# Optimization experiments

Hardware: AMD Instinct MI355X
Metric: run time of the kernel (lower is better)

Reference implementation:

```python
import jax, jax.numpy as jnp
import numpy as np

B, S, D = 2, 2048, 2048
H, KV = 16, 4
HD = D // H          # 128
QPK = H // KV        # queries per kv head


def setup_inputs() -> dict:
    key = jax.random.key(0)
    ks = jax.random.split(key, 8)
    x = jax.random.normal(ks[0], (B, S, D), jnp.float32)
    mask = jnp.zeros((1, 1, S, S), jnp.float32)  # unused (causal flash path)
    # RoPE tables: theta=10000, shape (S, HD//2)
    inv_freq = 1.0 / (10000.0 ** (jnp.arange(0, HD, 2, dtype=jnp.float32) / HD))
    freqs = jnp.outer(jnp.arange(S, dtype=jnp.float32), inv_freq)
    freqs_cos, freqs_sin = jnp.cos(freqs), jnp.sin(freqs)
    sc = 0.02
    Wq = jax.random.normal(ks[1], (D, H * HD), jnp.float32) * sc
    bq = jnp.zeros((H * HD,), jnp.float32)
    Wk = jax.random.normal(ks[2], (D, KV * HD), jnp.float32) * sc
    bk = jnp.zeros((KV * HD,), jnp.float32)
    Wv = jax.random.normal(ks[3], (D, KV * HD), jnp.float32) * sc
    bv = jnp.zeros((KV * HD,), jnp.float32)
    Wo = jax.random.normal(ks[4], (D, D), jnp.float32) * sc  # bias=False
    return dict(x=x, mask=mask, freqs_cos=freqs_cos, freqs_sin=freqs_sin,
                Wq=Wq, bq=bq, Wk=Wk, bk=bk, Wv=Wv, bv=bv, Wo=Wo)


def _rope(t, cos, sin):
    # t: [B, S, nH, HD]; interleaved-pair rotation as in apply_rope
    tr = t.reshape(t.shape[:-1] + (-1, 2))
    r, i = tr[..., 0], tr[..., 1]
    c = cos[None, :, None, :]
    s = sin[None, :, None, :]
    out = jnp.stack([r * c - i * s, r * s + i * c], axis=-1)
    return out.reshape(t.shape)


def reference(x, mask, freqs_cos, freqs_sin, Wq, bq, Wk, bk, Wv, bv, Wo):
    b, s, d = x.shape
    q = (x @ Wq + bq).reshape(b, s, H, HD)
    k = (x @ Wk + bk).reshape(b, s, KV, HD)
    v = (x @ Wv + bv).reshape(b, s, KV, HD)
    cos, sin = freqs_cos[:s], freqs_sin[:s]
    q = _rope(q, cos, sin)
    k = _rope(k, cos, sin)
    # GQA: repeat_interleave kv heads to match query heads
    k = jnp.repeat(k, QPK, axis=2)
    v = jnp.repeat(v, QPK, axis=2)
    q = q.transpose(0, 2, 1, 3)  # [B, H, S, HD]
    k = k.transpose(0, 2, 1, 3)
    v = v.transpose(0, 2, 1, 3)
    scores = jnp.einsum('bhqd,bhkd->bhqk', q, k) / jnp.sqrt(jnp.float32(HD))
    causal = jnp.tril(jnp.ones((s, s), bool))
    scores = jnp.where(causal[None, None], scores, jnp.finfo(scores.dtype).min)
    attn = jax.nn.softmax(scores, axis=-1)
    out = jnp.einsum('bhqk,bhkd->bhqd', attn, v)
    out = out.transpose(0, 2, 1, 3).reshape(b, s, d)
    return out @ Wo
```

## Files before the change

kernel.cpp:

```cpp
#include <hip/hip_runtime.h>


#define B_  2
#define S_  2048
#define D_  2048
#define H_  16
#define KV_ 4
#define HD_ 128
#define NQK 2560

typedef unsigned short ushort_t;
typedef __attribute__((ext_vector_type(8))) __bf16 bf16x8;
typedef __attribute__((ext_vector_type(4))) float  f32x4;

__device__ __forceinline__ ushort_t f2bf(float f) {
    unsigned u = __float_as_uint(f);
    u += 0x7FFFu + ((u >> 16) & 1u);
    return (ushort_t)(u >> 16);
}
__device__ __forceinline__ ushort_t f2bf_fast(float f) {
    __bf16 h = (__bf16)f;
    return *(ushort_t*)&h;
}
__device__ __forceinline__ float bf2f(ushort_t h) {
    return __uint_as_float(((unsigned)h) << 16);
}

__device__ __forceinline__ void g2l16(const void* g, void* l) {
    __builtin_amdgcn_global_load_lds(
        (const __attribute__((address_space(1))) unsigned int*)g,
        (__attribute__((address_space(3))) unsigned int*)l, 16, 0, 0);
}

#define SOFTSC 0.12751743f


__global__ __launch_bounds__(256) void k_prep(
    const float* __restrict__ x,  ushort_t* __restrict__ xb,
    const float* __restrict__ Wq, const float* __restrict__ Wk,
    const float* __restrict__ Wv, const float* __restrict__ Wo,
    ushort_t* __restrict__ Wt, ushort_t* __restrict__ Wot,
    const float* __restrict__ bq, const float* __restrict__ bk,
    const float* __restrict__ bv, float* __restrict__ bb) {
    __shared__ float tile[32][33];
    int id = blockIdx.x, t = threadIdx.x;
    if (id < 8192) {
        int i = id * 256 + t;
        float4 v = ((const float4*)x)[i];
        ushort4 o;
        o.x = f2bf(v.x); o.y = f2bf(v.y); o.z = f2bf(v.z); o.w = f2bf(v.w);
        ((ushort4*)xb)[i] = o;
        return;
    }
    const float* src; ushort_t* dst; int C, bid;
    if (id < 12288)      { src = Wq; dst = Wt;                       C = 2048; bid = id - 8192;  }
    else if (id < 13312) { src = Wk; dst = Wt + (size_t)2048 * 2048; C = 512;  bid = id - 12288; }
    else if (id < 14336) { src = Wv; dst = Wt + (size_t)2560 * 2048; C = 512;  bid = id - 13312; }
    else if (id < 18432) { src = Wo; dst = Wot;                      C = 2048; bid = id - 14336; }
    else {
        int i = (id - 18432) * 256 + t;
        if (i < 3072)
            bb[i] = (i < 2048) ? bq[i] : (i < 2560) ? bk[i - 2048] : bv[i - 2560];
        return;
    }
    const int R = 2048;
    int nbc = C >> 5;
    int c0 = (bid % nbc) * 32, r0 = (bid / nbc) * 32;
    int tx = t & 31, ty = t >> 5;
    for (int i = ty; i < 32; i += 8)
        tile[i][tx] = src[(size_t)(r0 + i) * C + c0 + tx];
    __syncthreads();
    for (int i = ty; i < 32; i += 8)
        dst[(size_t)(c0 + i) * R + r0 + tx] = f2bf(tile[tx][i]);
}


template<int BK>
__global__ __launch_bounds__(256, 3) void k_gemm(const ushort_t* __restrict__ A,
                                                 const ushort_t* __restrict__ Bt,
                                                 void* __restrict__ Cp,
                                                 const float* __restrict__ bias,
                                                 const float* __restrict__ fc,
                                                 const float* __restrict__ fs,
                                                 ushort_t* __restrict__ Vt,
                                                 int M, int N, int K, int out_bf16) {
    constexpr int GPR    = BK / 8;
    constexpr int RPR    = 64 / GPR;
    constexpr int ROUNDS = 32 / RPR;
    __shared__ __align__(16) ushort_t As[128 * BK];
    __shared__ __align__(16) ushort_t Bs[128 * BK];
    int t = threadIdx.x;
    int w = t >> 6, lane = t & 63, quad = lane >> 4, l16 = lane & 15;
    int L = blockIdx.x;
    int mper = (M >> 7) >> 3;
    int xcd = L & 7, j = L >> 3;
    int m0 = (xcd * mper + (j % mper)) * 128;
    int n0 = (j / mper) * 128;
    int wm = (w >> 1) * 64, wn = (w & 1) * 64;
    f32x4 acc[4][4] = {};

    int rlo = lane / GPR;
    int gsl = lane & (GPR - 1);
    const ushort_t* Ag = A  + (size_t)(m0 + w * 32) * K;
    const ushort_t* Bg = Bt + (size_t)(n0 + w * 32) * K;
    int rsw = (l16 & 7);

    for (int k0 = 0; k0 < K; k0 += BK) {
        __syncthreads();
#pragma unroll
        for (int p = 0; p < ROUNDS; p++) {
            int row = p * RPR + rlo;
            int gs = gsl ^ (row & 7);
            g2l16(Ag + (size_t)row * K + k0 + gs * 8, (char*)As + (w * 32 + p * RPR) * 2 * BK);
            g2l16(Bg + (size_t)row * K + k0 + gs * 8, (char*)Bs + (w * 32 + p * RPR) * 2 * BK);
        }
        __syncthreads();
#pragma unroll
        for (int kc = 0; kc < BK / 32; kc++) {
            int gg = quad + kc * 4;
            bf16x8 af[4], bfr[4];
#pragma unroll
            for (int i = 0; i < 4; i++)
                af[i] = *(const bf16x8*)(As + (wm + i * 16 + l16) * BK + ((gg ^ rsw) * 8));
#pragma unroll
            for (int j2 = 0; j2 < 4; j2++)
                bfr[j2] = *(const bf16x8*)(Bs + (wn + j2 * 16 + l16) * BK + ((gg ^ rsw) * 8));
#pragma unroll
            for (int i = 0; i < 4; i++)
#pragma unroll
                for (int j2 = 0; j2 < 4; j2++)
                    acc[i][j2] = __builtin_amdgcn_mfma_f32_16x16x32_bf16(af[i], bfr[j2], acc[i][j2], 0, 0, 0);
        }
    }
    int ostride = fc ? NQK : N;
#pragma unroll
    for (int i = 0; i < 4; i++) {
        int r = m0 + wm + i * 16 + quad * 4;
#pragma unroll
        for (int j2 = 0; j2 < 4; j2++) {
            int c = n0 + wn + j2 * 16 + l16;
            float bv_ = bias ? bias[c] : 0.f;
            if (fc && c >= 2560) {
                ushort4 pack;
                pack.x = f2bf(acc[i][j2][0] + bv_);
                pack.y = f2bf(acc[i][j2][1] + bv_);
                pack.z = f2bf(acc[i][j2][2] + bv_);
                pack.w = f2bf(acc[i][j2][3] + bv_);
                int kv = (c - 2560) >> 7, d = (c - 2560) & 127;
                int b = r >> 11, s0 = r & (S_ - 1);
                *(ushort4*)&Vt[(((size_t)b * KV_ + kv) * HD_ + d) * S_ + s0] = pack;
                continue;
            }
#pragma unroll
            for (int jr = 0; jr < 4; jr++) {
                float v = acc[i][j2][jr] + bv_;
                if (fc) {
                    int s  = (r + jr) & (S_ - 1);
                    int dp = (c & 127) >> 1;
                    float cs = fc[s * 64 + dp], sn = fs[s * 64 + dp];
                    float p = __shfl_xor(v, 1);
                    v = (c & 1) ? (v * cs + p * sn) : (v * cs - p * sn);
                }
                if (out_bf16) ((ushort_t*)Cp)[(size_t)(r + jr) * ostride + c] = f2bf(v);
                else          ((float*)Cp)[(size_t)(r + jr) * ostride + c] = v;
            }
        }
    }
}


#define G1_K  2048
#define G1_NT 32

__global__ __launch_bounds__(512, 2) void k_gemm1_256(
    const ushort_t* __restrict__ A, const ushort_t* __restrict__ Bt,
    ushort_t* __restrict__ C, const float* __restrict__ bias,
    const float* __restrict__ fc, const float* __restrict__ fs,
    ushort_t* __restrict__ Vt) {
    __shared__ __align__(16) ushort_t As[2][16384];
    __shared__ __align__(16) ushort_t Bs[2][12288];
    int t = threadIdx.x;
    int w = t >> 6, lane = t & 63, quad = lane >> 4, l16 = lane & 15;
    int wm_i = w >> 2, wn_i = w & 3;

    int L = blockIdx.x;
    int xcd = L & 7, j = L >> 3;
    int m0 = (xcd * 2 + (j & 1)) * 256;
    int n0 = (j >> 1) * 192;

    int srow = w * 16 + (lane >> 3);
    int sg   = (lane & 7) ^ (lane >> 3);
    const ushort_t* Ag  = A  + (size_t)(m0 + srow) * G1_K + sg * 8;
    const ushort_t* Bg3 = Bt + (size_t)(n0 + w * 8 + (lane >> 3)) * G1_K + sg * 8;

    int swz = l16 & 7;
    int cA = (quad ^ swz) * 8;
    int cB = ((quad + 4) ^ swz) * 8;

    f32x4 acc[8][3] = {};
    bf16x8 afr[4][2], bfr[3][2];

#define ST1A(KT, HA, BUF) do {                                                  \
    const ushort_t* s_ = Ag + (size_t)(HA) * 128 * G1_K + (KT) * 64;            \
    char* d_ = (char*)&As[BUF][(HA) * 8192] + w * 2048;                         \
    g2l16(s_, d_); g2l16(s_ + 8 * G1_K, d_ + 1024); } while (0)
#define ST1B(KT, G, BUF) do {                                                   \
    const ushort_t* s_ = Bg3 + (size_t)(G) * 64 * G1_K + (KT) * 64;             \
    char* d_ = (char*)&Bs[BUF][(G) * 4096] + w * 1024;                          \
    g2l16(s_, d_); } while (0)

#define RDA1(MH, BUF) do {                                                      \
    const ushort_t* Ar = &As[BUF][(wm_i * 128 + (MH) * 64 + l16) * 64];         \
    _Pragma("unroll") for (int ii = 0; ii < 4; ii++) {                          \
        afr[ii][0] = *(const bf16x8*)(Ar + ii * 1024 + cA);                     \
        afr[ii][1] = *(const bf16x8*)(Ar + ii * 1024 + cB); } } while (0)
#define RDB1(G, BUF) do {                                                       \
    const ushort_t* Br = &Bs[BUF][(wn_i * 48 + (G) * 16 + l16) * 64];           \
    bfr[G][0] = *(const bf16x8*)(Br + cA);                                      \
    bfr[G][1] = *(const bf16x8*)(Br + cB); } while (0)

#define MMA1(MH, G) do {                                                        \
    _Pragma("unroll") for (int kc = 0; kc < 2; kc++)                            \
    _Pragma("unroll") for (int ii = 0; ii < 4; ii++)                            \
        acc[(MH)*4+ii][G] = __builtin_amdgcn_mfma_f32_16x16x32_bf16(            \
            afr[ii][kc], bfr[G][kc], acc[(MH)*4+ii][G], 0, 0, 0); } while (0)

#define BAR1() __builtin_amdgcn_s_barrier()
#define WGK1() do { asm volatile("s_waitcnt lgkmcnt(0)" ::: "memory");          \
                    __builtin_amdgcn_sched_barrier(0); } while (0)

#define TILE1(KT, BUF, OTH) do {                                                \
                                                                        \
    RDA1(0, BUF); RDB1(0, BUF);                                                 \
    if ((KT) + 1 < G1_NT) ST1A((KT) + 1, 0, OTH);                               \
    BAR1(); WGK1();                                                             \
    __builtin_amdgcn_s_setprio(1); MMA1(0, 0); __builtin_amdgcn_s_setprio(0);   \
    BAR1();                                                                     \
                                                                        \
    RDB1(1, BUF); RDB1(2, BUF);                                                 \
    if ((KT) + 1 < G1_NT) ST1A((KT) + 1, 1, OTH);                               \
    BAR1(); WGK1();                                                             \
    __builtin_amdgcn_s_setprio(1); MMA1(0, 1); MMA1(0, 2);                      \
    __builtin_amdgcn_s_setprio(0);                                              \
    BAR1();                                                                     \
          \
    RDA1(1, BUF);                                                               \
    if ((KT) + 2 < G1_NT) { ST1B((KT) + 2, 0, BUF); ST1B((KT) + 2, 1, BUF); }   \
    BAR1(); WGK1();                                                             \
    __builtin_amdgcn_s_setprio(1); MMA1(1, 2); MMA1(1, 1);                      \
    __builtin_amdgcn_s_setprio(0);                                              \
    BAR1();                                                                     \
                              \
    if ((KT) + 2 < G1_NT) ST1B((KT) + 2, 2, BUF);                               \
    if ((KT) < G1_NT - 2) asm volatile("s_waitcnt vmcnt(3)" ::: "memory");      \
    else                  asm volatile("s_waitcnt vmcnt(0)" ::: "memory");      \
    BAR1();                                                                     \
    __builtin_amdgcn_sched_barrier(0);                                          \
    __builtin_amdgcn_s_setprio(1); MMA1(1, 0); __builtin_amdgcn_s_setprio(0);   \
    BAR1();                                                                     \
} while (0)

    ST1B(0, 0, 0); ST1B(0, 1, 0); ST1B(0, 2, 0);
    ST1A(0, 0, 0); ST1A(0, 1, 0);
    ST1B(1, 0, 1); ST1B(1, 1, 1); ST1B(1, 2, 1);
    asm volatile("s_waitcnt vmcnt(3)" ::: "memory");
    BAR1();

    for (int kt = 0; kt < G1_NT; kt += 2) {
        TILE1(kt, 0, 1);
        TILE1(kt + 1, 1, 0);
    }
#undef ST1A
#undef ST1B
#undef RDA1
#undef RDB1
#undef MMA1
#undef BAR1
#undef WGK1
#undef TILE1

#pragma unroll
    for (int i = 0; i < 8; i++) {
        int r = m0 + wm_i * 128 + i * 16 + quad * 4;
#pragma unroll
        for (int j2 = 0; j2 < 3; j2++) {
            int c = n0 + wn_i * 48 + j2 * 16 + l16;
            float bv_ = bias[c];
            if (c >= 2560) {
                ushort4 pack;
                pack.x = f2bf(acc[i][j2][0] + bv_);
                pack.y = f2bf(acc[i][j2][1] + bv_);
                pack.z = f2bf(acc[i][j2][2] + bv_);
                pack.w = f2bf(acc[i][j2][3] + bv_);
                int kv = (c - 2560) >> 7, d = (c - 2560) & 127;
                int b = r >> 11, s0 = r & (S_ - 1);
                *(ushort4*)&Vt[(((size_t)b * KV_ + kv) * HD_ + d) * S_ + s0] = pack;
                continue;
            }
#pragma unroll
            for (int jr = 0; jr < 4; jr++) {
                float v = acc[i][j2][jr] + bv_;
                int s  = (r + jr) & (S_ - 1);
                int dp = (c & 127) >> 1;
                float cs = fc[s * 64 + dp], sn = fs[s * 64 + dp];
                float p = __shfl_xor(v, 1);
                v = (c & 1) ? (v * cs + p * sn) : (v * cs - p * sn);
                if (c < 2048) v *= SOFTSC;
                C[(size_t)(r + jr) * NQK + c] = f2bf(v);
            }
        }
    }
}


__global__ __launch_bounds__(512, 4) void k_flash(const ushort_t* __restrict__ QK,
                                                  const ushort_t* __restrict__ Vt,
                                                  ushort_t* __restrict__ AO) {
    __shared__ __align__(16) ushort_t Ks[2 * 8192];
    __shared__ __align__(16) ushort_t Vs[2 * 8192];
    __shared__ __align__(16) ushort_t Ps[8 * 16 * 64];
    int h = blockIdx.y, b = blockIdx.z;
    int qt = b ? ((int)gridDim.x - 1 - (int)blockIdx.x) : (int)blockIdx.x;
    int kvh = h >> 2;
    int t = threadIdx.x, w = t >> 6, lane = t & 63, quad = lane >> 4, l16 = lane & 15;
    int qrow0 = qt * 128 + w * 16;

    bf16x8 aq[4];
    {
        const ushort_t* qb = QK + (size_t)(b * S_ + qrow0 + l16) * NQK + h * HD_ + quad * 8;
#pragma unroll
        for (int kc = 0; kc < 4; kc++) aq[kc] = *(const bf16x8*)(qb + kc * 32);
    }
    bf16x8 vone;
#pragma unroll
    for (int i = 0; i < 8; i++) vone[i] = (__bf16)1.0f;

    f32x4 o[8] = {};
    f32x4 ol = {};
    ushort_t* Psw = Ps + w * 16 * 64;
    int gsw = (l16 >> 1) & 3;

    const ushort_t* kgb = QK + (size_t)(b * S_) * NQK + 2048 + kvh * HD_;
    const ushort_t* vgb = Vt + ((size_t)(b * KV_ + kvh) * HD_) * S_;

    int sr, sgs; char *sK0, *sV0;
    if (t < 256) {
        sr = t >> 2; sgs = (t & 3) ^ ((sr >> 1) & 3);
        sK0 = (char*)Ks + (t >> 6) * 1024;
        sV0 = nullptr;
    } else {
        int u = t - 256;
        sr = u >> 2; sgs = (u & 3) ^ ((sr >> 1) & 3);
        sV0 = (char*)Vs + ((t - 256) >> 6) * 1024;
        sK0 = nullptr;
    }

#define STAGE(KT, BUF)                                                          \
    do {                                                                        \
        if (t < 256) {                                                          \
            const ushort_t* kg = kgb + (size_t)((KT) * 64 + sr) * NQK + sgs * 8; \
            char* KsW = sK0 + (BUF) * 16384;                                    \
            _Pragma("unroll")                                                   \
            for (int p = 0; p < 4; p++) g2l16(kg + p * 32, KsW + p * 4096);     \
        } else {                                                                \
            const ushort_t* vg = vgb + (KT) * 64 + sgs * 8 + (size_t)sr * S_;   \
            char* VsW = sV0 + (BUF) * 16384;                                    \
            _Pragma("unroll")                                                   \
            for (int p = 0; p < 4; p++)                                         \
                g2l16(vg + (size_t)((p & 1) * 64) * S_ + (p >> 1) * 32, VsW + p * 4096); \
        }                                                                       \
    } while (0)

    int ktmax = 2 * qt + 1;
    STAGE(0, 0);
    __syncthreads();

    for (int kt = 0; kt <= ktmax; kt++) {
        int cur = kt & 1;
        if (kt < ktmax) STAGE(kt + 1, cur ^ 1);

        if (kt * 64 <= qrow0 + 15) {
            const ushort_t* Kc = Ks + cur * 8192;
            const ushort_t* Vc = Vs + cur * 8192;
            f32x4 sacc[4] = {};
            __builtin_amdgcn_s_setprio(1);
#pragma unroll
            for (int kc = 0; kc < 4; kc++)
#pragma unroll
                for (int nb = 0; nb < 4; nb++) {
                    bf16x8 bk = *(const bf16x8*)(Kc + kc * 2048 + (nb * 16 + l16) * 32 + ((quad ^ gsw) * 8));
                    sacc[nb] = __builtin_amdgcn_mfma_f32_16x16x32_bf16(aq[kc], bk, sacc[nb], 0, 0, 0);
                }
            __builtin_amdgcn_s_setprio(0);
            if (kt * 64 + 63 > qrow0) {
#pragma unroll
                for (int nb = 0; nb < 4; nb++)
#pragma unroll
                    for (int jr = 0; jr < 4; jr++) {
                        int kcol = kt * 64 + nb * 16 + l16;
                        int qr = qrow0 + quad * 4 + jr;
                        if (kcol > qr) sacc[nb][jr] = -1e30f;
                    }
            }
#pragma unroll
            for (int nb = 0; nb < 4; nb++)
#pragma unroll
                for (int jr = 0; jr < 4; jr++) {
                    int q  = quad * 4 + jr;
                    int gi = (nb * 2 + (l16 >> 3)) ^ (q & 7);
                    Psw[q * 64 + gi * 8 + (l16 & 7)] = f2bf_fast(exp2f(sacc[nb][jr]));
                }

            asm volatile("s_waitcnt lgkmcnt(0)" ::: "memory");

            __builtin_amdgcn_s_setprio(1);
#pragma unroll
            for (int kc2 = 0; kc2 < 2; kc2++) {
                bf16x8 ap = *(const bf16x8*)(Psw + l16 * 64 + (((kc2 * 4 + quad) ^ (l16 & 7)) * 8));
                ol = __builtin_amdgcn_mfma_f32_16x16x32_bf16(ap, vone, ol, 0, 0, 0);
#pragma unroll
                for (int db = 0; db < 8; db++) {
                    bf16x8 bv = *(const bf16x8*)(Vc + kc2 * 4096 + (db * 16 + l16) * 32 + ((quad ^ gsw) * 8));
                    o[db] = __builtin_amdgcn_mfma_f32_16x16x32_bf16(ap, bv, o[db], 0, 0, 0);
                }
            }
            __builtin_amdgcn_s_setprio(0);
        }
        __syncthreads();
    }
#undef STAGE

#pragma unroll
    for (int jr = 0; jr < 4; jr++) {
        float inv = 1.0f / ol[jr];
        size_t rbase = (size_t)(b * S_ + qrow0 + quad * 4 + jr) * D_ + h * HD_;
#pragma unroll
        for (int db = 0; db < 8; db++)
            AO[rbase + db * 16 + l16] = f2bf(o[db][jr] * inv);
    }
}


extern "C" void kernel_launch(void* const* d_in, const int* in_sizes, int n_in,
                              void* d_out, int out_size, void* d_ws, size_t ws_size,
                              hipStream_t stream) {
    const float* x  = (const float*)d_in[0];
    const float* fc = (const float*)d_in[2];
    const float* fs = (const float*)d_in[3];
    const float* Wq = (const float*)d_in[4];
    const float* bq = (const float*)d_in[5];
    const float* Wk = (const float*)d_in[6];
    const float* bk = (const float*)d_in[7];
    const float* Wv = (const float*)d_in[8];
    const float* bv = (const float*)d_in[9];
    const float* Wo = (const float*)d_in[10];

    char* ws = (char*)d_ws;
    ushort_t* xb  = (ushort_t*)(ws);
    ushort_t* Wt  = (ushort_t*)(ws + 16777216);
    ushort_t* Wot = (ushort_t*)(ws + 29360128);
    float*    bb  = (float*)   (ws + 37748736);
    ushort_t* QK  = (ushort_t*)(ws + 37761024);
    ushort_t* Vt  = (ushort_t*)(ws + 58732544);
    ushort_t* AO  = xb;
    float* out = (float*)d_out;

    k_prep<<<18444, 256, 0, stream>>>(x, xb, Wq, Wk, Wv, Wo, Wt, Wot, bq, bk, bv, bb);
    k_gemm1_256<<<256, 512, 0, stream>>>(xb, Wt, QK, bb, fc, fs, Vt);
    k_flash<<<dim3(16, 16, 2), 512, 0, stream>>>(QK, Vt, AO);
    k_gemm<128><<<512, 256, 0, stream>>>(AO, Wot, out, nullptr, nullptr, nullptr, nullptr,
                                         4096, 2048, 2048, 0);
}
```

Before: 304.2 us.

## Software-pipeline LDS fragment reads across MFMA phases in QKV GEMM

Restructures the QKV projection GEMM main loop so LDS-to-register fragment loads for the next phase, and the next k-tile's first A/B fragments, are issued before the current MFMAs run. Double-buffered fragment registers replace the full lgkmcnt(0) waits with partial counts. It also drops several barriers per tile. This is meant to hide LDS read latency behind matrix-core work, at the cost of extra VGPRs (possible occupancy or spill pressure) and subtler ordering between LDS writes and reads.

New measurement: 303.6 us. About the same (-0.2%).

```diff
diff --git a/kernel.cpp b/kernel.cpp
--- a/kernel.cpp
+++ b/kernel.cpp
@@ -198,7 +198,9 @@
     int cB = ((quad + 4) ^ swz) * 8;
 
     f32x4 acc[8][3] = {};
-    bf16x8 afr[4][2], bfr[3][2];
+    bf16x8 afr0[4][2], afr1[4][2];
+    bf16x8 b0a[2], b0b[2];
+    bf16x8 b1[2], b2[2];
 
 #define ST1A(KT, HA, BUF) do {                                                  \
     const ushort_t* s_ = Ag + (size_t)(HA) * 128 * G1_K + (KT) * 64;            \
@@ -209,55 +211,55 @@
     char* d_ = (char*)&Bs[BUF][(G) * 4096] + w * 1024;                          \
     g2l16(s_, d_); } while (0)
 
-#define RDA1(MH, BUF) do {                                                      \
+#define RDA_TO(DST, MH, BUF) do {                                               \
     const ushort_t* Ar = &As[BUF][(wm_i * 128 + (MH) * 64 + l16) * 64];         \
     _Pragma("unroll") for (int ii = 0; ii < 4; ii++) {                          \
-        afr[ii][0] = *(const bf16x8*)(Ar + ii * 1024 + cA);                     \
-        afr[ii][1] = *(const bf16x8*)(Ar + ii * 1024 + cB); } } while (0)
-#define RDB1(G, BUF) do {                                                       \
+        DST[ii][0] = *(const bf16x8*)(Ar + ii * 1024 + cA);                     \
+        DST[ii][1] = *(const bf16x8*)(Ar + ii * 1024 + cB); } } while (0)
+#define RDB_TO(DST, G, BUF) do {                                                \
     const ushort_t* Br = &Bs[BUF][(wn_i * 48 + (G) * 16 + l16) * 64];           \
-    bfr[G][0] = *(const bf16x8*)(Br + cA);                                      \
-    bfr[G][1] = *(const bf16x8*)(Br + cB); } while (0)
-
-#define MMA1(MH, G) do {                                                        \
+    DST[0] = *(const bf16x8*)(Br + cA);                                         \
+    DST[1] = *(const bf16x8*)(Br + cB); } while (0)
+
+#define MMA1(AFR, MH, BF, G) do {                                               \
     _Pragma("unroll") for (int kc = 0; kc < 2; kc++)                            \
     _Pragma("unroll") for (int ii = 0; ii < 4; ii++)                            \
         acc[(MH)*4+ii][G] = __builtin_amdgcn_mfma_f32_16x16x32_bf16(            \
-            afr[ii][kc], bfr[G][kc], acc[(MH)*4+ii][G], 0, 0, 0); } while (0)
+            AFR[ii][kc], BF[kc], acc[(MH)*4+ii][G], 0, 0, 0); } while (0)
 
 #define BAR1() __builtin_amdgcn_s_barrier()
-#define WGK1() do { asm volatile("s_waitcnt lgkmcnt(0)" ::: "memory");          \
-                    __builtin_amdgcn_sched_barrier(0); } while (0)
-
-#define TILE1(KT, BUF, OTH) do {                                                \
-                                                                        \
-    RDA1(0, BUF); RDB1(0, BUF);                                                 \
+#define LGKM(N) do { asm volatile("s_waitcnt lgkmcnt(" #N ")" ::: "memory");    \
+                     __builtin_amdgcn_sched_barrier(0); } while (0)
+
+#define TILE1(KT, BUF, OTH, B0C, B0N) do {                                      \
+                          \
     if ((KT) + 1 < G1_NT) ST1A((KT) + 1, 0, OTH);                               \
-    BAR1(); WGK1();                                                             \
-    __builtin_amdgcn_s_setprio(1); MMA1(0, 0); __builtin_amdgcn_s_setprio(0);   \
     BAR1();                                                                     \
-                                                                        \
-    RDB1(1, BUF); RDB1(2, BUF);                                                 \
+    RDB_TO(b1, 1, BUF); RDB_TO(b2, 2, BUF);                                     \
+    LGKM(4);                                                                    \
+    __builtin_amdgcn_s_setprio(1); MMA1(afr0, 0, B0C, 0);                       \
+    __builtin_amdgcn_s_setprio(0);                                              \
+                     \
     if ((KT) + 1 < G1_NT) ST1A((KT) + 1, 1, OTH);                               \
-    BAR1(); WGK1();                                                             \
-    __builtin_amdgcn_s_setprio(1); MMA1(0, 1); MMA1(0, 2);                      \
+    BAR1();                                                                     \
+    RDA_TO(afr1, 1, BUF);                                                       \
+    LGKM(8);                                                                    \
+    __builtin_amdgcn_s_setprio(1); MMA1(afr0, 0, b1, 1); MMA1(afr0, 0, b2, 2);  \
     __builtin_amdgcn_s_setprio(0);                                              \
+                 \
+    if ((KT) + 2 < G1_NT) { ST1B((KT) + 2, 0, BUF); ST1B((KT) + 2, 1, BUF); }   \
     BAR1();                                                                     \
-          \
-    RDA1(1, BUF);                                                               \
-    if ((KT) + 2 < G1_NT) { ST1B((KT) + 2, 0, BUF); ST1B((KT) + 2, 1, BUF); }   \
-    BAR1(); WGK1();                                                             \
-    __builtin_amdgcn_s_setprio(1); MMA1(1, 2); MMA1(1, 1);                      \
+    LGKM(0);                                                                    \
+    __builtin_amdgcn_s_setprio(1); MMA1(afr1, 1, b2, 2); MMA1(afr1, 1, b1, 1);  \
     __builtin_amdgcn_s_setprio(0);                                              \
-    BAR1();                                                                     \
-                              \
+     \
     if ((KT) + 2 < G1_NT) ST1B((KT) + 2, 2, BUF);                               \
     if ((KT) < G1_NT - 2) asm volatile("s_waitcnt vmcnt(3)" ::: "memory");      \
     else                  asm volatile("s_waitcnt vmcnt(0)" ::: "memory");      \
     BAR1();                                                                     \
-    __builtin_amdgcn_sched_barrier(0);                                          \
-    __builtin_amdgcn_s_setprio(1); MMA1(1, 0); __builtin_amdgcn_s_setprio(0);   \
-    BAR1();                                                                     \
+    if ((KT) + 1 < G1_NT) { RDA_TO(afr0, 0, OTH); RDB_TO(B0N, 0, OTH); }        \
+    __builtin_amdgcn_s_setprio(1); MMA1(afr1, 1, B0C, 0);                       \
+    __builtin_amdgcn_s_setprio(0);                                              \
 } while (0)
 
     ST1B(0, 0, 0); ST1B(0, 1, 0); ST1B(0, 2, 0);
@@ -265,18 +267,19 @@
     ST1B(1, 0, 1); ST1B(1, 1, 1); ST1B(1, 2, 1);
     asm volatile("s_waitcnt vmcnt(3)" ::: "memory");
     BAR1();
+    RDA_TO(afr0, 0, 0); RDB_TO(b0a, 0, 0);
 
     for (int kt = 0; kt < G1_NT; kt += 2) {
-        TILE1(kt, 0, 1);
-        TILE1(kt + 1, 1, 0);
+        TILE1(kt, 0, 1, b0a, b0b);
+        TILE1(kt + 1, 1, 0, b0b, b0a);
     }
 #undef ST1A
 #undef ST1B
-#undef RDA1
-#undef RDB1
+#undef RDA_TO
+#undef RDB_TO
 #undef MMA1
 #undef BAR1
-#undef WGK1
+#undef LGKM
 #undef TILE1
 
 #pragma unroll
```

## Shrink QKV GEMM tile to 128x192 and simplify double-buffered pipeline

Applied to the files above, without the earlier changes.

The fused QKV projection GEMM moves from 256x192 tiles with 256 blocks to 128x192 tiles with 512 blocks. Accumulator count halves and shared memory shrinks, and the launch bound is raised to 4 blocks per CU to improve occupancy. The inner pipeline is restructured to prefetch the next K-tile into the other buffer with fewer barriers. In exchange, arithmetic intensity per tile drops and global loads of B rise, and the vmcnt-based sync is looser, which could expose latency.

New measurement: 302.6 us. No clear change (-0.5%).

```diff
diff --git a/kernel.cpp b/kernel.cpp
--- a/kernel.cpp
+++ b/kernel.cpp
@@ -172,12 +172,12 @@
 #define G1_K  2048
 #define G1_NT 32
 
-__global__ __launch_bounds__(512, 2) void k_gemm1_256(
+__global__ __launch_bounds__(512, 4) void k_gemm1_256(
     const ushort_t* __restrict__ A, const ushort_t* __restrict__ Bt,
     ushort_t* __restrict__ C, const float* __restrict__ bias,
     const float* __restrict__ fc, const float* __restrict__ fs,
     ushort_t* __restrict__ Vt) {
-    __shared__ __align__(16) ushort_t As[2][16384];
+    __shared__ __align__(16) ushort_t As[2][8192];
     __shared__ __align__(16) ushort_t Bs[2][12288];
     int t = threadIdx.x;
     int w = t >> 6, lane = t & 63, quad = lane >> 4, l16 = lane & 15;
@@ -185,103 +185,93 @@
 
     int L = blockIdx.x;
     int xcd = L & 7, j = L >> 3;
-    int m0 = (xcd * 2 + (j & 1)) * 256;
-    int n0 = (j >> 1) * 192;
-
-    int srow = w * 16 + (lane >> 3);
+    int m0 = (xcd * 4 + (j & 3)) * 128;
+    int n0 = (j >> 2) * 192;
+
+    int srow = w * 8 + (lane >> 3);
     int sg   = (lane & 7) ^ (lane >> 3);
     const ushort_t* Ag  = A  + (size_t)(m0 + srow) * G1_K + sg * 8;
-    const ushort_t* Bg3 = Bt + (size_t)(n0 + w * 8 + (lane >> 3)) * G1_K + sg * 8;
+    const ushort_t* Bg3 = Bt + (size_t)(n0 + srow) * G1_K + sg * 8;
 
     int swz = l16 & 7;
     int cA = (quad ^ swz) * 8;
     int cB = ((quad + 4) ^ swz) * 8;
 
-    f32x4 acc[8][3] = {};
-    bf16x8 afr[4][2], bfr[3][2];
-
-#define ST1A(KT, HA, BUF) do {                                                  \
-    const ushort_t* s_ = Ag + (size_t)(HA) * 128 * G1_K + (KT) * 64;            \
-    char* d_ = (char*)&As[BUF][(HA) * 8192] + w * 2048;                         \
-    g2l16(s_, d_); g2l16(s_ + 8 * G1_K, d_ + 1024); } while (0)
-#define ST1B(KT, G, BUF) do {                                                   \
+    f32x4 acc[4][3] = {};
+    bf16x8 afr[4][2], bf_[2];
+
+#define ST_A(KT, HA, BUF) do {                                                  \
+    const ushort_t* s_ = Ag + (size_t)(HA) * 64 * G1_K + (KT) * 64;             \
+    char* d_ = (char*)&As[BUF][(HA) * 4096] + w * 1024;                         \
+    g2l16(s_, d_); } while (0)
+#define ST_B(KT, G, BUF) do {                                                   \
     const ushort_t* s_ = Bg3 + (size_t)(G) * 64 * G1_K + (KT) * 64;             \
     char* d_ = (char*)&Bs[BUF][(G) * 4096] + w * 1024;                          \
     g2l16(s_, d_); } while (0)
 
-#define RDA1(MH, BUF) do {                                                      \
-    const ushort_t* Ar = &As[BUF][(wm_i * 128 + (MH) * 64 + l16) * 64];         \
+#define RDA(BUF) do {                                                           \
+    const ushort_t* Ar = &As[BUF][(wm_i * 64 + l16) * 64];                      \
     _Pragma("unroll") for (int ii = 0; ii < 4; ii++) {                          \
         afr[ii][0] = *(const bf16x8*)(Ar + ii * 1024 + cA);                     \
         afr[ii][1] = *(const bf16x8*)(Ar + ii * 1024 + cB); } } while (0)
-#define RDB1(G, BUF) do {                                                       \
+#define RDB(G, BUF) do {                                                        \
     const ushort_t* Br = &Bs[BUF][(wn_i * 48 + (G) * 16 + l16) * 64];           \
-    bfr[G][0] = *(const bf16x8*)(Br + cA);                                      \
-    bfr[G][1] = *(const bf16x8*)(Br + cB); } while (0)
-
-#define MMA1(MH, G) do {                                                        \
+    bf_[0] = *(const bf16x8*)(Br + cA);                                         \
+    bf_[1] = *(const bf16x8*)(Br + cB); } while (0)
+
+#define MMA(G) do {                                                             \
     _Pragma("unroll") for (int kc = 0; kc < 2; kc++)                            \
     _Pragma("unroll") for (int ii = 0; ii < 4; ii++)                            \
-        acc[(MH)*4+ii][G] = __builtin_amdgcn_mfma_f32_16x16x32_bf16(            \
-            afr[ii][kc], bfr[G][kc], acc[(MH)*4+ii][G], 0, 0, 0); } while (0)
+        acc[ii][G] = __builtin_amdgcn_mfma_f32_16x16x32_bf16(                   \
+            afr[ii][kc], bf_[kc], acc[ii][G], 0, 0, 0); } while (0)
 
 #define BAR1() __builtin_amdgcn_s_barrier()
-#define WGK1() do { asm volatile("s_waitcnt lgkmcnt(0)" ::: "memory");          \
-                    __builtin_amdgcn_sched_barrier(0); } while (0)
-
-#define TILE1(KT, BUF, OTH) do {                                                \
+#define LGKM0() do { asm volatile("s_waitcnt lgkmcnt(0)" ::: "memory");         \
+                     __builtin_amdgcn_sched_barrier(0); } while (0)
+
+#define TILE(KT, BUF, OTH) do {                                                 \
                                                                         \
-    RDA1(0, BUF); RDB1(0, BUF);                                                 \
-    if ((KT) + 1 < G1_NT) ST1A((KT) + 1, 0, OTH);                               \
-    BAR1(); WGK1();                                                             \
-    __builtin_amdgcn_s_setprio(1); MMA1(0, 0); __builtin_amdgcn_s_setprio(0);   \
-    BAR1();                                                                     \
+    if ((KT) + 1 < G1_NT) { ST_A((KT) + 1, 0, OTH); ST_B((KT) + 1, 0, OTH); }   \
+    RDA(BUF); RDB(0, BUF);                                                      \
+    LGKM0();                                                                    \
+    __builtin_amdgcn_s_setprio(1); MMA(0); __builtin_amdgcn_s_setprio(0);       \
                                                                         \
-    RDB1(1, BUF); RDB1(2, BUF);                                                 \
-    if ((KT) + 1 < G1_NT) ST1A((KT) + 1, 1, OTH);                               \
-    BAR1(); WGK1();                                                             \
-    __builtin_amdgcn_s_setprio(1); MMA1(0, 1); MMA1(0, 2);                      \
-    __builtin_amdgcn_s_setprio(0);                                              \
-    BAR1();                                                                     \
-          \
-    RDA1(1, BUF);                                                               \
-    if ((KT) + 2 < G1_NT) { ST1B((KT) + 2, 0, BUF); ST1B((KT) + 2, 1, BUF); }   \
-    BAR1(); WGK1();                                                             \
-    __builtin_amdgcn_s_setprio(1); MMA1(1, 2); MMA1(1, 1);                      \
-    __builtin_amdgcn_s_setprio(0);                                              \
-    BAR1();                                                                     \
-                              \
-    if ((KT) + 2 < G1_NT) ST1B((KT) + 2, 2, BUF);                               \
-    if ((KT) < G1_NT - 2) asm volatile("s_waitcnt vmcnt(3)" ::: "memory");      \
+    if ((KT) + 1 < G1_NT) { ST_A((KT) + 1, 1, OTH); ST_B((KT) + 1, 1, OTH); }   \
+    RDB(1, BUF);                                                                \
+    LGKM0();                                                                    \
+    __builtin_amdgcn_s_setprio(1); MMA(1); __builtin_amdgcn_s_setprio(0);       \
+                                                                        \
+    if ((KT) + 1 < G1_NT) ST_B((KT) + 1, 2, OTH);                               \
+    if ((KT) + 1 < G1_NT) asm volatile("s_waitcnt vmcnt(1)" ::: "memory");      \
     else                  asm volatile("s_waitcnt vmcnt(0)" ::: "memory");      \
     BAR1();                                                                     \
-    __builtin_amdgcn_sched_barrier(0);                                          \
-    __builtin_amdgcn_s_setprio(1); MMA1(1, 0); __builtin_amdgcn_s_setprio(0);   \
+    RDB(2, BUF);                                                                \
+    LGKM0();                                                                    \
+    __builtin_amdgcn_s_setprio(1); MMA(2); __builtin_amdgcn_s_setprio(0);       \
     BAR1();                                                                     \
 } while (0)
 
-    ST1B(0, 0, 0); ST1B(0, 1, 0); ST1B(0, 2, 0);
-    ST1A(0, 0, 0); ST1A(0, 1, 0);
-    ST1B(1, 0, 1); ST1B(1, 1, 1); ST1B(1, 2, 1);
-    asm volatile("s_waitcnt vmcnt(3)" ::: "memory");
+    ST_A(0, 0, 0); ST_A(0, 1, 0);
+    ST_B(0, 0, 0); ST_B(0, 1, 0); ST_B(0, 2, 0);
+    asm volatile("s_waitcnt vmcnt(0)" ::: "memory");
     BAR1();
 
     for (int kt = 0; kt < G1_NT; kt += 2) {
-        TILE1(kt, 0, 1);
-        TILE1(kt + 1, 1, 0);
-    }
-#undef ST1A
-#undef ST1B
-#undef RDA1
-#undef RDB1
-#undef MMA1
+        TILE(kt, 0, 1);
+        TILE(kt + 1, 1, 0);
+    }
+#undef ST_A
+#undef ST_B
+#undef RDA
+#undef RDB
+#undef MMA
 #undef BAR1
-#undef WGK1
-#undef TILE1
-
-#pragma unroll
-    for (int i = 0; i < 8; i++) {
-        int r = m0 + wm_i * 128 + i * 16 + quad * 4;
+#undef LGKM0
+#undef TILE
+
+#pragma unroll
+    for (int i = 0; i < 4; i++) {
+        int r = m0 + wm_i * 64 + i * 16 + quad * 4;
 #pragma unroll
         for (int j2 = 0; j2 < 3; j2++) {
             int c = n0 + wn_i * 48 + j2 * 16 + l16;
@@ -466,7 +456,7 @@
     float* out = (float*)d_out;
 
     k_prep<<<18444, 256, 0, stream>>>(x, xb, Wq, Wk, Wv, Wo, Wt, Wot, bq, bk, bv, bb);
-    k_gemm1_256<<<256, 512, 0, stream>>>(xb, Wt, QK, bb, fc, fs, Vt);
+    k_gemm1_256<<<512, 512, 0, stream>>>(xb, Wt, QK, bb, fc, fs, Vt);
     k_flash<<<dim3(16, 16, 2), 512, 0, stream>>>(QK, Vt, AO);
     k_gemm<128><<<512, 256, 0, stream>>>(AO, Wot, out, nullptr, nullptr, nullptr, nullptr,
                                          4096, 2048, 2048, 0);
```
